# Kernel optimization log

Hardware: AMD Instinct MI355X
Metric: run time of the kernel (lower is better)

## Reference

```python
import jax, jax.numpy as jnp
import numpy as np
from jax import lax


def conv3x3(x, w):
    # x: (B,C,H,W), w: (O,I,3,3); stride 1, padding 1, no bias
    return lax.conv_general_dilated(x, w, (1, 1), 'SAME',
                                    dimension_numbers=('NCHW', 'OIHW', 'NCHW'))


def group_norm(x, w, b, groups=32, eps=1e-5):
    B, C, H, W = x.shape
    xg = x.reshape(B, groups, C // groups, H, W)
    mu = xg.mean(axis=(2, 3, 4), keepdims=True)
    var = xg.var(axis=(2, 3, 4), keepdims=True)
    xg = (xg - mu) * lax.rsqrt(var + eps)
    return xg.reshape(B, C, H, W) * w[None, :, None, None] + b[None, :, None, None]


def to_patches(x, p1, p2):
    # 'b c (h p1) (w p2) -> (b h w) c (p1 p2)'
    B, C, H, W = x.shape
    h, w = H // p1, W // p2
    x = x.reshape(B, C, h, p1, w, p2).transpose(0, 2, 4, 1, 3, 5)
    return x.reshape(B * h * w, C, p1 * p2)


def from_patches(x, B, h, w, p1, p2):
    # '(b h w) c (p1 p2) -> b c (h p1) (w p2)'
    C = x.shape[1]
    x = x.reshape(B, h, w, C, p1, p2).transpose(0, 3, 1, 4, 2, 5)
    return x.reshape(B, C, h * p1, w * p2)


def setup_inputs() -> dict:
    key = jax.random.key(0)
    ks = jax.random.split(key, 5)
    B, C, H, W = 8, 256, 128, 128
    inter = 256
    s = 0.05  # keep conv outputs in a sane range
    return {
        'x_low': jax.random.normal(ks[0], (B, C, H, W), jnp.float32),
        'x_high': jax.random.normal(ks[1], (B, C, H, W), jnp.float32),
        'w_q': jax.random.normal(ks[2], (inter, C, 3, 3), jnp.float32) * s,
        'gq_w': jnp.ones((inter,), jnp.float32),
        'gq_b': jnp.zeros((inter,), jnp.float32),
        'w_k': jax.random.normal(ks[3], (inter, C, 3, 3), jnp.float32) * s,
        'gk_w': jnp.ones((inter,), jnp.float32),
        'gk_b': jnp.zeros((inter,), jnp.float32),
        'w_o': jax.random.normal(ks[4], (C, inter, 3, 3), jnp.float32) * s,
        'go_w': jnp.ones((C,), jnp.float32),
        'go_b': jnp.zeros((C,), jnp.float32),
        'p1': 8,
        'p2': 8,
    }


def reference(x_low, x_high, w_q, gq_w, gq_b, w_k, gk_w, gk_b, w_o, go_w, go_b, p1, p2):
    B, C, H, W = x_low.shape
    inter = w_q.shape[0]
    h, w = H // p1, W // p2
    # q, k: (B*h*w, inter, T) with T = p1*p2
    q = to_patches(group_norm(conv3x3(x_low, w_q), gq_w, gq_b), p1, p2)
    k = to_patches(group_norm(conv3x3(x_high, w_k), gk_w, gk_b), p1, p2)
    q = q.transpose(0, 2, 1)                                  # (N, T, inter)
    attn = jnp.matmul(q, k) / jnp.sqrt(jnp.float32(inter))    # (N, T, T)
    attn = jax.nn.softmax(attn, axis=-1)
    out = jnp.matmul(attn, k.transpose(0, 2, 1))              # (N, T, inter)
    out = from_patches(out.transpose(0, 2, 1), B, h, w, p1, p2)
    return group_norm(conv3x3(out + x_low, w_o), go_w, go_b)
```

## Files before the change

### kernel.cpp

```cpp
#include <hip/hip_runtime.h>

using u16 = unsigned short;
using u32 = unsigned int;

typedef short bfrag8 __attribute__((ext_vector_type(8)));
typedef float f32x4  __attribute__((ext_vector_type(4)));

__device__ __forceinline__ void unpack8(const int4 v, float f[8]) {
  u32 a = (u32)v.x, b = (u32)v.y, c = (u32)v.z, d = (u32)v.w;
  f[0] = __uint_as_float(a << 16);
  f[1] = __uint_as_float(a & 0xffff0000u);
  f[2] = __uint_as_float(b << 16);
  f[3] = __uint_as_float(b & 0xffff0000u);
  f[4] = __uint_as_float(c << 16);
  f[5] = __uint_as_float(c & 0xffff0000u);
  f[6] = __uint_as_float(d << 16);
  f[7] = __uint_as_float(d & 0xffff0000u);
}

__device__ __forceinline__ u16 f2bf(float f) {
  u32 u = __float_as_uint(f);
  u32 r = u + 0x7fffu + ((u >> 16) & 1u);
  return (u16)(r >> 16);
}

__device__ __forceinline__ void gload_lds16(const void* g, void* l) {
  __builtin_amdgcn_global_load_lds(
      (const __attribute__((address_space(1))) void*)g,
      (__attribute__((address_space(3))) void*)l, 16, 0, 0);
}

__global__ __launch_bounds__(256) void wprep(
    const float* __restrict__ wq, const float* __restrict__ wk, const float* __restrict__ wo,
    u16* __restrict__ dq, u16* __restrict__ dk, u16* __restrict__ dwo)
{
  const float* s = (blockIdx.y == 0) ? wq : (blockIdx.y == 1) ? wk : wo;
  u16* d = (blockIdx.y == 0) ? dq : (blockIdx.y == 1) ? dk : dwo;
  int id = blockIdx.x * 256 + threadIdx.x;
  int e = id * 4;
  int tap = e >> 16;
  int rem = e & 65535;
  int oc = rem >> 8, ic = rem & 255;
  u16 o[4];
#pragma unroll
  for (int j = 0; j < 4; ++j)
    o[j] = f2bf(s[((size_t)oc * 256 + ic + j) * 9 + tap]);
  *reinterpret_cast<uint2*>(d + e) = *reinterpret_cast<uint2*>(o);
}

__global__ __launch_bounds__(256) void xpose(
    const float* __restrict__ xa, const float* __restrict__ xb,
    u16* __restrict__ oa, u16* __restrict__ ob)
{
  const int row = blockIdx.x, b = blockIdx.y;
  const float* src = blockIdx.z ? xb : xa;
  u16* dst = blockIdx.z ? ob : oa;
  const int t = threadIdx.x;
  const int px4 = (t >> 3) * 4;
  const int c8 = (t & 7) * 8;
#pragma unroll
  for (int p = 0; p < 4; ++p) {
    int c0 = p * 64 + c8;
    float4 v[8];
#pragma unroll
    for (int j = 0; j < 8; ++j)
      v[j] = *reinterpret_cast<const float4*>(src + ((size_t)b * 256 + c0 + j) * 16384 + row * 128 + px4);
#pragma unroll
    for (int e = 0; e < 4; ++e) {
      u16 o[8];
      o[0] = f2bf(e==0?v[0].x:e==1?v[0].y:e==2?v[0].z:v[0].w);
      o[1] = f2bf(e==0?v[1].x:e==1?v[1].y:e==2?v[1].z:v[1].w);
      o[2] = f2bf(e==0?v[2].x:e==1?v[2].y:e==2?v[2].z:v[2].w);
      o[3] = f2bf(e==0?v[3].x:e==1?v[3].y:e==2?v[3].z:v[3].w);
      o[4] = f2bf(e==0?v[4].x:e==1?v[4].y:e==2?v[4].z:v[4].w);
      o[5] = f2bf(e==0?v[5].x:e==1?v[5].y:e==2?v[5].z:v[5].w);
      o[6] = f2bf(e==0?v[6].x:e==1?v[6].y:e==2?v[6].z:v[6].w);
      o[7] = f2bf(e==0?v[7].x:e==1?v[7].y:e==2?v[7].z:v[7].w);
      *reinterpret_cast<int4*>(dst + (((size_t)b * 128 + row) * 128 + px4 + e) * 256 + c0) =
          *reinterpret_cast<int4*>(o);
    }
  }
}

__global__ __launch_bounds__(512, 4) void conv_mfma(
    const u16* __restrict__ X, const u16* __restrict__ W2, u16* __restrict__ Y,
    float* __restrict__ part)
{
  __shared__ __attribute__((aligned(16))) char csm[71680];

  const int t = threadIdx.x;
  const int l = t & 63;
  const int wv = t >> 6;
  const int id = blockIdx.x;
  const int u = (id & 7) * 128 + (id >> 3);
  const int bb = u >> 7, y0 = u & 127;
  const int och = wv >> 1, pxh = wv & 1;
  const int lc = l & 15, lq = l >> 4;

  f32x4 acc[4][4];
#pragma unroll
  for (int m = 0; m < 4; ++m)
#pragma unroll
    for (int n = 0; n < 4; ++n) acc[m][n] = (f32x4){0.f, 0.f, 0.f, 0.f};

  const size_t xplane = (size_t)bb * (128 * 128 * 256);

  {
    int4 z = {0, 0, 0, 0};
    if (t < 24) {
      int q = t & 3, sel = (t >> 2) & 1, kh = t >> 3;
      int cidx = sel ? 129 : 0;
      *reinterpret_cast<int4*>(csm + ((kh * 132 + cidx) * 4 + q) * 16) = z;
    }
    if (y0 == 0)
      for (int s = t; s < 528; s += 512) *reinterpret_cast<int4*>(csm + s * 16) = z;
    if (y0 == 127)
      for (int s = t; s < 528; s += 512) *reinterpret_cast<int4*>(csm + 16896 + s * 16) = z;
  }

  auto stageA = [&](int tap, int buf, int ic0) {
#pragma unroll
    for (int i = 0; i < 2; ++i) {
      int idx = t + i * 512;
      const u16* src = W2 + (((size_t)(tap * 256 + (idx >> 2))) << 8) + ic0 + (idx & 3) * 8;
      gload_lds16(src, csm + 25344 + buf * 16384 + (i * 512 + (t & ~63)) * 16);
    }
  };
  auto stageB = [&](int ic0) {
#pragma unroll
    for (int i = 0; i < 3; ++i) {
      int idx = t + i * 512;
      int kh = idx >> 9;
      int row = y0 - 1 + kh;
      if (row >= 0 && row < 128) {
        int px = (idx & 511) >> 2, q = idx & 3;
        const u16* src = X + xplane + (((size_t)(row * 128 + px)) << 8) + ic0 + q * 8;
        gload_lds16(src, csm + 64 + kh * 256 + (i * 512 + (t & ~63)) * 16);
      }
    }
  };

  stageB(0);
  stageA(0, 0, 0);
  __syncthreads();

  for (int chunk = 0; chunk < 8; ++chunk) {
    const int ic0 = chunk * 32;
#pragma unroll
    for (int tap = 0; tap < 9; ++tap) {
      const int kh = tap / 3, kw = tap % 3, buf = tap & 1;
      if (tap < 8) stageA(tap + 1, buf ^ 1, ic0);
      bfrag8 af[4], xf[4];
#pragma unroll
      for (int m = 0; m < 4; ++m)
        af[m] = *reinterpret_cast<const bfrag8*>(csm + 25344 + buf * 16384 +
                    ((och * 64 + m * 16 + lc) * 4 + lq) * 16);
#pragma unroll
      for (int n = 0; n < 4; ++n)
        xf[n] = *reinterpret_cast<const bfrag8*>(csm + kh * 8448 + kw * 64 +
                    ((pxh * 64 + n * 16 + lc) * 64 + lq * 16));
#pragma unroll
      for (int m = 0; m < 4; ++m)
#pragma unroll
        for (int n = 0; n < 4; ++n)
          acc[m][n] = __builtin_amdgcn_mfma_f32_16x16x32_bf16(af[m], xf[n], acc[m][n], 0, 0, 0);
      __syncthreads();
    }
    if (chunk < 7) {
      stageB(ic0 + 32);
      stageA(0, 0, ic0 + 32);
      __syncthreads();
    }
  }

  u16* Ost = (u16*)csm;
  float* sst = (float*)(csm + 67584);
  const int chb = och * 64 + lq * 4;
  const int pxb = pxh * 64 + lc;
#pragma unroll
  for (int m = 0; m < 4; ++m)
#pragma unroll
    for (int n = 0; n < 4; ++n) {
      u32 lo = (u32)f2bf(acc[m][n][0]) | ((u32)f2bf(acc[m][n][1]) << 16);
      u32 hi = (u32)f2bf(acc[m][n][2]) | ((u32)f2bf(acc[m][n][3]) << 16);
      uint2 pk = {lo, hi};
      *reinterpret_cast<uint2*>(&Ost[(pxb + n * 16) * 264 + chb + m * 16]) = pk;
    }
#pragma unroll
  for (int m = 0; m < 4; ++m)
#pragma unroll
    for (int r = 0; r < 4; ++r) {
      float s  = acc[m][0][r] + acc[m][1][r] + acc[m][2][r] + acc[m][3][r];
      float ss = acc[m][0][r] * acc[m][0][r] + acc[m][1][r] * acc[m][1][r] +
                 acc[m][2][r] * acc[m][2][r] + acc[m][3][r] * acc[m][3][r];
#pragma unroll
      for (int off = 1; off < 16; off <<= 1) {
        s  += __shfl_xor(s, off);
        ss += __shfl_xor(ss, off);
      }
      if (lc == 0) {
        int c = och * 64 + m * 16 + lq * 4 + r;
        sst[pxh * 512 + c]       = s;
        sst[pxh * 512 + 256 + c] = ss;
      }
    }
  __syncthreads();

  if (t < 256) {
    float s  = sst[t]       + sst[512 + t];
    float ss = sst[256 + t] + sst[768 + t];
    size_t pb = (((size_t)bb * 128 + y0) * 256 + t) * 2;
    part[pb]     = s;
    part[pb + 1] = ss;
  }
#pragma unroll
  for (int s8 = 0; s8 < 8; ++s8) {
    int pix = s8 * 16 + (t >> 5);
    int sub = t & 31;
    int4 v = *reinterpret_cast<const int4*>(&Ost[pix * 264 + sub * 8]);
    *reinterpret_cast<int4*>(Y + xplane + (((size_t)(y0 * 128 + pix)) << 8) + sub * 8) = v;
  }
}

__global__ __launch_bounds__(256) void gnstat2b(const float* __restrict__ part, float* __restrict__ stat)
{
  const int b = blockIdx.x, t = threadIdx.x;
  float s = 0.f, ss = 0.f;
  for (int row = 0; row < 128; ++row) {
    size_t pb = (((size_t)b * 128 + row) * 256 + t) * 2;
    s  += part[pb];
    ss += part[pb + 1];
  }
  __shared__ float Ls[256], Lss[256];
  Ls[t] = s; Lss[t] = ss;
  __syncthreads();
  if (t < 32) {
    float S = 0.f, SS = 0.f;
#pragma unroll
    for (int j = 0; j < 8; ++j) { S += Ls[t * 8 + j]; SS += Lss[t * 8 + j]; }
    float mean = S * (1.f / 131072.f);
    float var = SS * (1.f / 131072.f) - mean * mean;
    stat[b * 32 + t] = mean;
    stat[256 + b * 32 + t] = rsqrtf(var + 1e-5f);
  }
}

__global__ __launch_bounds__(256) void normkT(
    const u16* __restrict__ yk, const float* __restrict__ statk,
    const float* __restrict__ gkw, const float* __restrict__ gkb,
    u16* __restrict__ kT)
{
  __shared__ u16 L[8][264];
  const int y = blockIdx.x, b = blockIdx.y;
  const int ph = y >> 3, py = y & 7;
  const int t = threadIdx.x;
  const int px = t >> 5, c8 = (t & 31) * 8;
  const int g = c8 >> 3;
  float mean = statk[b * 32 + g], rstd = statk[256 + b * 32 + g];
  float A[8], Bv[8];
#pragma unroll
  for (int j = 0; j < 8; ++j) {
    A[j] = rstd * gkw[c8 + j];
    Bv[j] = gkb[c8 + j] - mean * A[j];
  }
  const size_t rowbase = (((size_t)b * 128 + y) * 128) * 256;
  const size_t outbase = ((size_t)(b * 16 + ph) * 8 + py) * 32768;
  for (int pw = 0; pw < 16; ++pw) {
    int4 v = *reinterpret_cast<const int4*>(yk + rowbase + (size_t)(pw * 8 + px) * 256 + c8);
    float f[8]; unpack8(v, f);
    u16 o[8];
#pragma unroll
    for (int j = 0; j < 8; ++j) o[j] = f2bf(f[j] * A[j] + Bv[j]);
    *reinterpret_cast<int4*>(&L[px][c8]) = *reinterpret_cast<int4*>(o);
    __syncthreads();
    u16 o2[8];
#pragma unroll
    for (int q = 0; q < 8; ++q) o2[q] = L[q][t];
    *reinterpret_cast<int4*>(kT + outbase + (size_t)(pw * 256 + t) * 8) = *reinterpret_cast<int4*>(o2);
    __syncthreads();
  }
}

#define OST 280
__global__ __launch_bounds__(256, 3) void attn_mfma(
    const u16* __restrict__ yq, const u16* __restrict__ yk,
    const u16* __restrict__ kT, const u16* __restrict__ xl,
    const float* __restrict__ statq, const float* __restrict__ statk,
    const float* __restrict__ gqw, const float* __restrict__ gqb,
    const float* __restrict__ gkw,
    u16* __restrict__ resid)
{
  __shared__ __attribute__((aligned(16))) u16 smem[64 * OST + 4 * 16 * 72];
  u16* Ost = smem;
  u16* Pls = smem + 64 * OST;

  const int n = blockIdx.x;
  const int b = n >> 8, ph = (n >> 4) & 15, pw = n & 15;
  const int t = threadIdx.x, l = t & 63, w = t >> 6;
  const int lc = l & 15, lg = l >> 4;

  auto tokaddr = [&](int tok) -> size_t {
    return (((size_t)(b * 128 + ph * 8 + (tok >> 3))) * 128 + pw * 8 + (tok & 7)) * 256;
  };

  const size_t qa = tokaddr(16 * w + lc) + lg * 8;
  bfrag8 aF[8];
#pragma unroll
  for (int ks = 0; ks < 8; ++ks) {
    int c0 = lg * 8 + ks * 32;
    int g = ks * 4 + lg;
    float meanq = statq[b * 32 + g], rstdq = statq[256 + b * 32 + g];
    float rstdk = statk[256 + b * 32 + g];
    int4 v = *reinterpret_cast<const int4*>(yq + qa + ks * 32);
    float f[8]; unpack8(v, f);
    float4 w0 = *reinterpret_cast<const float4*>(gqw + c0);
    float4 w1 = *reinterpret_cast<const float4*>(gqw + c0 + 4);
    float4 b0 = *reinterpret_cast<const float4*>(gqb + c0);
    float4 b1 = *reinterpret_cast<const float4*>(gqb + c0 + 4);
    float4 k0 = *reinterpret_cast<const float4*>(gkw + c0);
    float4 k1 = *reinterpret_cast<const float4*>(gkw + c0 + 4);
    float ww[8] = {w0.x, w0.y, w0.z, w0.w, w1.x, w1.y, w1.z, w1.w};
    float bb[8] = {b0.x, b0.y, b0.z, b0.w, b1.x, b1.y, b1.z, b1.w};
    float kk[8] = {k0.x, k0.y, k0.z, k0.w, k1.x, k1.y, k1.z, k1.w};
    u16 o[8];
#pragma unroll
    for (int j = 0; j < 8; ++j) {
      float Aq = rstdq * ww[j];
      float Bq = bb[j] - meanq * Aq;
      float Ak = rstdk * kk[j];
      o[j] = f2bf((f[j] * Aq + Bq) * Ak);
    }
    aF[ks] = *reinterpret_cast<bfrag8*>(o);
  }

  f32x4 sacc[4];
#pragma unroll
  for (int nt = 0; nt < 4; ++nt) sacc[nt] = (f32x4){0.f, 0.f, 0.f, 0.f};

#pragma unroll
  for (int nt = 0; nt < 4; ++nt) {
    const size_t ka = tokaddr(nt * 16 + lc) + lg * 8;
    bfrag8 bF[8];
#pragma unroll
    for (int ks = 0; ks < 8; ++ks)
      bF[ks] = *reinterpret_cast<const bfrag8*>(yk + ka + ks * 32);
#pragma unroll
    for (int ks = 0; ks < 8; ++ks)
      sacc[nt] = __builtin_amdgcn_mfma_f32_16x16x32_bf16(aF[ks], bF[ks], sacc[nt], 0, 0, 0);
  }

  u16* Pw = Pls + w * (16 * 72);
#pragma unroll
  for (int r = 0; r < 4; ++r) {
    float m0 = fmaxf(fmaxf(sacc[0][r], sacc[1][r]), fmaxf(sacc[2][r], sacc[3][r]));
    m0 = fmaxf(m0, __shfl_xor(m0, 1));
    m0 = fmaxf(m0, __shfl_xor(m0, 2));
    m0 = fmaxf(m0, __shfl_xor(m0, 4));
    m0 = fmaxf(m0, __shfl_xor(m0, 8));
    float p0 = __expf((sacc[0][r] - m0) * 0.0625f);
    float p1 = __expf((sacc[1][r] - m0) * 0.0625f);
    float p2 = __expf((sacc[2][r] - m0) * 0.0625f);
    float p3 = __expf((sacc[3][r] - m0) * 0.0625f);
    float s0 = p0 + p1 + p2 + p3;
    s0 += __shfl_xor(s0, 1);
    s0 += __shfl_xor(s0, 2);
    s0 += __shfl_xor(s0, 4);
    s0 += __shfl_xor(s0, 8);
    float inv = 1.f / s0;
    int prow = (lg * 4 + r) * 72;
    Pw[prow + 0 * 16 + lc] = f2bf(p0 * inv);
    Pw[prow + 1 * 16 + lc] = f2bf(p1 * inv);
    Pw[prow + 2 * 16 + lc] = f2bf(p2 * inv);
    Pw[prow + 3 * 16 + lc] = f2bf(p3 * inv);
  }

  bfrag8 pA[2];
#pragma unroll
  for (int js = 0; js < 2; ++js)
    pA[js] = *reinterpret_cast<const bfrag8*>(Pw + lc * 72 + js * 32 + lg * 8);

  f32x4 pacc[16];
#pragma unroll
  for (int ct = 0; ct < 16; ++ct) pacc[ct] = (f32x4){0.f, 0.f, 0.f, 0.f};

#pragma unroll
  for (int ct = 0; ct < 16; ++ct) {
    bfrag8 vB[2];
#pragma unroll
    for (int js = 0; js < 2; ++js)
      vB[js] = *reinterpret_cast<const bfrag8*>(
          kT + ((size_t)((b * 16 + ph) * 8 + js * 4 + lg)) * 32768 +
          (size_t)(pw * 256 + ct * 16 + lc) * 8);
#pragma unroll
    for (int js = 0; js < 2; ++js)
      pacc[ct] = __builtin_amdgcn_mfma_f32_16x16x32_bf16(pA[js], vB[js], pacc[ct], 0, 0, 0);
  }

#pragma unroll
  for (int ct = 0; ct < 16; ++ct)
#pragma unroll
    for (int r = 0; r < 4; ++r)
      Ost[(16 * w + lg * 4 + r) * OST + ct * 16 + lc] = f2bf(pacc[ct][r]);
  __syncthreads();

#pragma unroll
  for (int s = 0; s < 8; ++s) {
    int px_ = t >> 5;
    int c16 = t & 31;
    size_t g = (((size_t)b * 128 + ph * 8 + s) * 128 + pw * 8 + px_) * 256 + c16 * 8;
    int4 o = *reinterpret_cast<const int4*>(&Ost[(s * 8 + px_) * OST + c16 * 8]);
    int4 r = *reinterpret_cast<const int4*>(xl + g);
    float fo[8], fr[8]; unpack8(o, fo); unpack8(r, fr);
    u16 pk[8];
#pragma unroll
    for (int j = 0; j < 8; ++j) pk[j] = f2bf(fo[j] + fr[j]);
    *reinterpret_cast<int4*>(resid + g) = *reinterpret_cast<int4*>(pk);
  }
}

__global__ __launch_bounds__(256) void gnapply_t(
    const u16* __restrict__ Y, const float* __restrict__ stat,
    const float* __restrict__ gw, const float* __restrict__ gb,
    float* __restrict__ out)
{
  const int row = blockIdx.x, b = blockIdx.y;
  const int t = threadIdx.x;
  const int px4 = (t & 31) * 4;
  const int c8 = (t >> 5) * 8;
#pragma unroll
  for (int p = 0; p < 4; ++p) {
    int c0 = p * 64 + c8;
    int g = c0 >> 3;
    float mean = stat[b * 32 + g], rstd = stat[256 + b * 32 + g];
    float A[8], Bv[8];
#pragma unroll
    for (int j = 0; j < 8; ++j) {
      A[j] = rstd * gw[c0 + j];
      Bv[j] = gb[c0 + j] - mean * A[j];
    }
    float vals[4][8];
#pragma unroll
    for (int e = 0; e < 4; ++e) {
      int4 v = *reinterpret_cast<const int4*>(Y + (((size_t)b * 128 + row) * 128 + px4 + e) * 256 + c0);
      float f[8]; unpack8(v, f);
#pragma unroll
      for (int j = 0; j < 8; ++j) vals[e][j] = fmaf(f[j], A[j], Bv[j]);
    }
#pragma unroll
    for (int j = 0; j < 8; ++j) {
      float4 o = {vals[0][j], vals[1][j], vals[2][j], vals[3][j]};
      *reinterpret_cast<float4*>(out + ((size_t)b * 256 + c0 + j) * 16384 + row * 128 + px4) = o;
    }
  }
}

extern "C" void kernel_launch(void* const* d_in, const int* in_sizes, int n_in,
                              void* d_out, int out_size, void* d_ws, size_t ws_size,
                              hipStream_t stream)
{
  const float* x_low  = (const float*)d_in[0];
  const float* x_high = (const float*)d_in[1];
  const float* w_q    = (const float*)d_in[2];
  const float* gq_w   = (const float*)d_in[3];
  const float* gq_b   = (const float*)d_in[4];
  const float* w_k    = (const float*)d_in[5];
  const float* gk_w   = (const float*)d_in[6];
  const float* gk_b   = (const float*)d_in[7];
  const float* w_o    = (const float*)d_in[8];
  const float* go_w   = (const float*)d_in[9];
  const float* go_b   = (const float*)d_in[10];
  float* out = (float*)d_out;

  char* ws = (char*)d_ws;
  const size_t slot = 67108864;
  u16* xl  = (u16*)(ws + 0 * slot);
  u16* xh  = (u16*)(ws + 1 * slot);
  u16* yq  = (u16*)(ws + 2 * slot);
  u16* yk  = (u16*)(ws + 3 * slot);
  u16* kT  = (u16*)(ws + 4 * slot);
  u16* W2q = (u16*)(ws + 5 * slot);
  u16* W2k = W2q + 589824;
  u16* W2o = W2k + 589824;
  float* partq = (float*)(ws + 5 * slot + 3 * 1179648);
  float* partk = partq + 524288;
  float* parto = partk + 524288;
  float* statq = parto + 524288;
  float* statk = statq + 512;
  float* stato = statk + 512;

  wprep<<<dim3(576, 3), 256, 0, stream>>>(w_q, w_k, w_o, W2q, W2k, W2o);
  xpose<<<dim3(128, 8, 2), 256, 0, stream>>>(x_low, x_high, xl, xh);
  conv_mfma<<<1024, 512, 0, stream>>>(xl, W2q, yq, partq);
  conv_mfma<<<1024, 512, 0, stream>>>(xh, W2k, yk, partk);
  gnstat2b<<<8, 256, 0, stream>>>(partq, statq);
  gnstat2b<<<8, 256, 0, stream>>>(partk, statk);
  normkT<<<dim3(128, 8), 256, 0, stream>>>(yk, statk, gk_w, gk_b, kT);
  attn_mfma<<<2048, 256, 0, stream>>>(yq, yk, kT, xl, statq, statk,
                                      gq_w, gq_b, gk_w, xh);
  conv_mfma<<<1024, 512, 0, stream>>>(xh, W2o, xl, parto);
  gnstat2b<<<8, 256, 0, stream>>>(parto, stato);
  gnapply_t<<<dim3(128, 8), 256, 0, stream>>>(xl, stato, go_w, go_b, out);
}
```

Measured before the change: 693.7 us.

## Triple-buffer conv weight taps, swizzle LDS reads, and use fine-grained waitcnt barriers

The conv kernel's weight staging moves from double to triple buffering, so tap loads are issued two taps ahead. A per-block __syncthreads after the MFMAs is replaced by explicit lgkmcnt/vmcnt waits plus a raw s_barrier placed before the MFMAs. LDS addresses for both the weight and input tiles are XOR-swizzled to cut bank conflicts, and MFMA issue gets raised priority. The changes raise LDS use, which may lower occupancy, and the hand-counted vmcnt values must match the number of outstanding loads exactly or the reads become racy.

```diff
diff --git a/kernel.cpp b/kernel.cpp
--- a/kernel.cpp
+++ b/kernel.cpp
@@ -86,7 +86,7 @@
     const u16* __restrict__ X, const u16* __restrict__ W2, u16* __restrict__ Y,
     float* __restrict__ part)
 {
-  __shared__ __attribute__((aligned(16))) char csm[71680];
+  __shared__ __attribute__((aligned(16))) char csm[74496];
 
   const int t = threadIdx.x;
   const int l = t & 63;
@@ -96,6 +96,7 @@
   const int bb = u >> 7, y0 = u & 127;
   const int och = wv >> 1, pxh = wv & 1;
   const int lc = l & 15, lq = l >> 4;
+  const int sa = (lc >> 1) & 3;
 
   f32x4 acc[4][4];
 #pragma unroll
@@ -122,7 +123,9 @@
 #pragma unroll
     for (int i = 0; i < 2; ++i) {
       int idx = t + i * 512;
-      const u16* src = W2 + (((size_t)(tap * 256 + (idx >> 2))) << 8) + ic0 + (idx & 3) * 8;
+      int oc = idx >> 2, q = idx & 3;
+      int qs = q ^ ((oc >> 1) & 3);
+      const u16* src = W2 + (((size_t)(tap * 256 + oc)) << 8) + ic0 + qs * 8;
       gload_lds16(src, csm + 25344 + buf * 16384 + (i * 512 + (t & ~63)) * 16);
     }
   };
@@ -134,7 +137,8 @@
       int row = y0 - 1 + kh;
       if (row >= 0 && row < 128) {
         int px = (idx & 511) >> 2, q = idx & 3;
-        const u16* src = X + xplane + (((size_t)(row * 128 + px)) << 8) + ic0 + q * 8;
+        int qs = q ^ (((px + 1) >> 1) & 3);
+        const u16* src = X + xplane + (((size_t)(row * 128 + px)) << 8) + ic0 + qs * 8;
         gload_lds16(src, csm + 64 + kh * 256 + (i * 512 + (t & ~63)) * 16);
       }
     }
@@ -142,33 +146,50 @@
 
   stageB(0);
   stageA(0, 0, 0);
+  stageA(1, 1, 0);
   __syncthreads();
 
   for (int chunk = 0; chunk < 8; ++chunk) {
     const int ic0 = chunk * 32;
 #pragma unroll
     for (int tap = 0; tap < 9; ++tap) {
-      const int kh = tap / 3, kw = tap % 3, buf = tap & 1;
-      if (tap < 8) stageA(tap + 1, buf ^ 1, ic0);
+      const int kh = tap / 3, kw = tap % 3, buf = tap % 3;
+      if (tap <= 6) stageA(tap + 2, (tap + 2) % 3, ic0);
+
       bfrag8 af[4], xf[4];
+      const int sb = ((lc + kw) >> 1) & 3;
 #pragma unroll
       for (int m = 0; m < 4; ++m)
         af[m] = *reinterpret_cast<const bfrag8*>(csm + 25344 + buf * 16384 +
-                    ((och * 64 + m * 16 + lc) * 4 + lq) * 16);
-#pragma unroll
-      for (int n = 0; n < 4; ++n)
-        xf[n] = *reinterpret_cast<const bfrag8*>(csm + kh * 8448 + kw * 64 +
-                    ((pxh * 64 + n * 16 + lc) * 64 + lq * 16));
+                    (((och * 64 + m * 16 + lc) * 4) + (lq ^ sa)) * 16);
+#pragma unroll
+      for (int n = 0; n < 4; ++n) {
+        int S = pxh * 64 + n * 16 + lc + kw;
+        xf[n] = *reinterpret_cast<const bfrag8*>(csm + kh * 8448 + S * 64 + (lq ^ sb) * 16);
+      }
+      asm volatile("s_waitcnt lgkmcnt(0)" ::: "memory");
+      __builtin_amdgcn_sched_barrier(0);
+      if (tap <= 6) {
+        asm volatile("s_waitcnt vmcnt(2)" ::: "memory");
+      } else if (tap == 7) {
+        asm volatile("s_waitcnt vmcnt(0)" ::: "memory");
+      }
+      __builtin_amdgcn_sched_barrier(0);
+      __builtin_amdgcn_s_barrier();
+      __builtin_amdgcn_sched_barrier(0);
+
+      __builtin_amdgcn_s_setprio(1);
 #pragma unroll
       for (int m = 0; m < 4; ++m)
 #pragma unroll
         for (int n = 0; n < 4; ++n)
           acc[m][n] = __builtin_amdgcn_mfma_f32_16x16x32_bf16(af[m], xf[n], acc[m][n], 0, 0, 0);
-      __syncthreads();
+      __builtin_amdgcn_s_setprio(0);
     }
     if (chunk < 7) {
+      stageA(0, 0, ic0 + 32);
+      stageA(1, 1, ic0 + 32);
       stageB(ic0 + 32);
-      stageA(0, 0, ic0 + 32);
       __syncthreads();
     }
   }
```

Measured after the change: 692.3 us. About the same (-0.2%).
